# Performance work log

Hardware: AMD Instinct MI355X
Metric: run time of the kernel (lower is better)

The kernel has to match this reference:

```python
import jax, jax.numpy as jnp
import numpy as np

EPS = 1e-12  # matches torch F.normalize eps


def _l2_normalize(x, axis=-1):
    # torch.F.normalize: x / max(||x||, eps)
    n = jnp.sqrt(jnp.sum(x * x, axis=axis, keepdims=True))
    return x / jnp.maximum(n, EPS)


def setup_inputs() -> dict:
    N, n_classes, embed_dim = 32768, 1000, 1024
    key = jax.random.key(0)
    k_feat, k_lab, k_proto = jax.random.split(key, 3)

    features = jax.random.normal(k_feat, (N, embed_dim), dtype=jnp.float32)

    # one-hot float labels, as expected by `torch.matmul(labels, self.mean_class)`
    y = jax.random.randint(k_lab, (N,), 0, n_classes)
    labels = jax.nn.one_hot(y, n_classes, dtype=jnp.float32)

    # predefined prototypes: orthonormal rows (ortho_group.rvs equivalent via QR)
    g = jax.random.normal(k_proto, (embed_dim, embed_dim), dtype=jnp.float32)
    q, _ = jnp.linalg.qr(g)
    mean_class = q[:n_classes]  # [n_classes, embed_dim], orthonormal rows

    return {"features": features, "labels": labels, "mean_class": mean_class}


def reference(features, labels, mean_class):
    # features: [N, D]; labels: [N, C] one-hot; mean_class: [C, D]
    # (3-D feature mean-pooling branch not exercised: inputs are 2-D)
    proto_y = labels @ mean_class                 # [N, D]
    f = _l2_normalize(features, axis=1)
    p = _l2_normalize(proto_y, axis=1)
    # diag(f @ p.T) == rowwise dot product -> same math, O(N*D) not O(N^2*D)
    cos = jnp.einsum("nd,nd->n", f, p)            # [N]
    return jnp.mean(1.0 - cos)
```

## Files before the change

kernel.cpp:

```cpp
#include <hip/hip_runtime.h>

constexpr int N_CLASSES = 1000;
constexpr int EMBED     = 1024;

typedef float floatx4 __attribute__((ext_vector_type(4)));

__global__ __launch_bounds__(256) void angular_rows_kernel(
    const float* __restrict__ features,
    const float* __restrict__ labels,
    const float* __restrict__ mean_class,
    float* __restrict__ partials,
    int n_rows)
{
    const int tid  = threadIdx.x;
    const int lane = tid & 63;
    const int wave = tid >> 6;
    const int row  = blockIdx.x * 4 + wave;

    float res = 0.0f;

    if (row < n_rows) {
        const floatx4* frow = (const floatx4*)(features + (size_t)row * EMBED);
        floatx4 f0 = __builtin_nontemporal_load(frow + lane);
        floatx4 f1 = __builtin_nontemporal_load(frow + lane + 64);
        floatx4 f2 = __builtin_nontemporal_load(frow + lane + 128);
        floatx4 f3 = __builtin_nontemporal_load(frow + lane + 192);

        const floatx4* lrow = (const floatx4*)(labels + (size_t)row * N_CLASSES);
        floatx4 l0 = __builtin_nontemporal_load(lrow + lane);
        floatx4 l1 = __builtin_nontemporal_load(lrow + lane + 64);
        floatx4 l2 = __builtin_nontemporal_load(lrow + lane + 128);
        floatx4 l3 = (lane < N_CLASSES / 4 - 192)
                         ? __builtin_nontemporal_load(lrow + lane + 192)
                         : (floatx4){0.f, 0.f, 0.f, 0.f};

        int cand = -1;
        if (l0.x != 0.f) cand = 4 * lane + 0;
        if (l0.y != 0.f) cand = 4 * lane + 1;
        if (l0.z != 0.f) cand = 4 * lane + 2;
        if (l0.w != 0.f) cand = 4 * lane + 3;
        if (l1.x != 0.f) cand = 4 * (lane + 64) + 0;
        if (l1.y != 0.f) cand = 4 * (lane + 64) + 1;
        if (l1.z != 0.f) cand = 4 * (lane + 64) + 2;
        if (l1.w != 0.f) cand = 4 * (lane + 64) + 3;
        if (l2.x != 0.f) cand = 4 * (lane + 128) + 0;
        if (l2.y != 0.f) cand = 4 * (lane + 128) + 1;
        if (l2.z != 0.f) cand = 4 * (lane + 128) + 2;
        if (l2.w != 0.f) cand = 4 * (lane + 128) + 3;
        if (l3.x != 0.f) cand = 4 * (lane + 192) + 0;
        if (l3.y != 0.f) cand = 4 * (lane + 192) + 1;
        if (l3.z != 0.f) cand = 4 * (lane + 192) + 2;
        if (l3.w != 0.f) cand = 4 * (lane + 192) + 3;

        unsigned long long m = __ballot(cand >= 0);
        int src = __ffsll((unsigned long long)m) - 1;
        int cls = __shfl(cand, src, 64);
        cls = __builtin_amdgcn_readfirstlane(cls);

        const floatx4* prow = (const floatx4*)(mean_class + (size_t)cls * EMBED);
        floatx4 p0 = prow[lane];
        floatx4 p1 = prow[lane + 64];
        floatx4 p2 = prow[lane + 128];
        floatx4 p3 = prow[lane + 192];

        float ff = 0.f, pp = 0.f, fp = 0.f;
        #define DOT3(F, P) \
            ff += F.x*F.x + F.y*F.y + F.z*F.z + F.w*F.w; \
            pp += P.x*P.x + P.y*P.y + P.z*P.z + P.w*P.w; \
            fp += F.x*P.x + F.y*P.y + F.z*P.z + F.w*P.w;
        DOT3(f0, p0) DOT3(f1, p1) DOT3(f2, p2) DOT3(f3, p3)
        #undef DOT3

        #pragma unroll
        for (int msk = 1; msk < 64; msk <<= 1) {
            ff += __shfl_xor(ff, msk, 64);
            pp += __shfl_xor(pp, msk, 64);
            fp += __shfl_xor(fp, msk, 64);
        }
        const float denom = fmaxf(sqrtf(ff), 1e-12f) * fmaxf(sqrtf(pp), 1e-12f);
        res = 1.0f - fp / denom;
    }

    __shared__ float s_red[4];
    if (lane == 0) s_red[wave] = res;
    __syncthreads();
    if (tid == 0)
        partials[blockIdx.x] = s_red[0] + s_red[1] + s_red[2] + s_red[3];
}

__global__ __launch_bounds__(256) void reduce_partials_kernel(
    const float* __restrict__ partials, int num_partials,
    float* __restrict__ out, float inv_n)
{
    const int tid  = threadIdx.x;
    const int lane = tid & 63;
    const int wave = tid >> 6;
    __shared__ float s_red[4];

    float acc = 0.0f;
    for (int i = tid; i < num_partials; i += 256)
        acc += partials[i];
    #pragma unroll
    for (int msk = 1; msk < 64; msk <<= 1)
        acc += __shfl_xor(acc, msk, 64);
    if (lane == 0) s_red[wave] = acc;
    __syncthreads();
    if (tid == 0)
        out[0] = (s_red[0] + s_red[1] + s_red[2] + s_red[3]) * inv_n;
}

extern "C" void kernel_launch(void* const* d_in, const int* in_sizes, int n_in,
                              void* d_out, int out_size, void* d_ws, size_t ws_size,
                              hipStream_t stream) {
    const float* features   = (const float*)d_in[0];
    const float* labels     = (const float*)d_in[1];
    const float* mean_class = (const float*)d_in[2];
    float* out = (float*)d_out;
    float* partials = (float*)d_ws;

    const int n_rows = in_sizes[0] / EMBED;
    const int num_blocks = (n_rows + 3) / 4;

    angular_rows_kernel<<<num_blocks, 256, 0, stream>>>(
        features, labels, mean_class, partials, n_rows);
    reduce_partials_kernel<<<1, 256, 0, stream>>>(
        partials, num_blocks, out, 1.0f / (float)n_rows);
}
```

Before: 260.5 us.

## Split label class scan into separate kernel before dot-product kernel

Moves the one-hot label scan into its own kernel, with one block per row, that writes each row's class index to a workspace buffer. The dot-product kernel then reads that index and can issue the prototype loads alongside the feature loads, instead of waiting on the label load, ballot and shuffle chain. The cost is an extra kernel launch, a 32768-block grid in which 6 of every 256 threads sit idle, and a round trip of the index buffer through memory. If a label row is all zeros, its cls_buf entry is never written and holds whatever was left in the workspace.

```diff
diff --git a/kernel.cpp b/kernel.cpp
--- a/kernel.cpp
+++ b/kernel.cpp
@@ -5,10 +5,29 @@
 
 typedef float floatx4 __attribute__((ext_vector_type(4)));
 
-__global__ __launch_bounds__(256) void angular_rows_kernel(
+__global__ __launch_bounds__(256) void class_scan_kernel(
+    const float* __restrict__ labels,
+    int* __restrict__ cls_buf)
+{
+    const int row = blockIdx.x;
+    const int t   = threadIdx.x;
+    if (t < N_CLASSES / 4) {
+        const floatx4* lrow = (const floatx4*)(labels + (size_t)row * N_CLASSES);
+        floatx4 v = __builtin_nontemporal_load(lrow + t);
+        if (v.x != 0.f || v.y != 0.f || v.z != 0.f || v.w != 0.f) {
+            int c = 4 * t;
+            if      (v.y != 0.f) c += 1;
+            else if (v.z != 0.f) c += 2;
+            else if (v.w != 0.f) c += 3;
+            cls_buf[row] = c;
+        }
+    }
+}
+
+__global__ __launch_bounds__(256) void angular_dots_kernel(
     const float* __restrict__ features,
-    const float* __restrict__ labels,
     const float* __restrict__ mean_class,
+    const int* __restrict__ cls_buf,
     float* __restrict__ partials,
     int n_rows)
 {
@@ -20,44 +39,15 @@
     float res = 0.0f;
 
     if (row < n_rows) {
+        const int cls = __builtin_amdgcn_readfirstlane(cls_buf[row]);
+
         const floatx4* frow = (const floatx4*)(features + (size_t)row * EMBED);
+        const floatx4* prow = (const floatx4*)(mean_class + (size_t)cls * EMBED);
+
         floatx4 f0 = __builtin_nontemporal_load(frow + lane);
         floatx4 f1 = __builtin_nontemporal_load(frow + lane + 64);
         floatx4 f2 = __builtin_nontemporal_load(frow + lane + 128);
         floatx4 f3 = __builtin_nontemporal_load(frow + lane + 192);
-
-        const floatx4* lrow = (const floatx4*)(labels + (size_t)row * N_CLASSES);
-        floatx4 l0 = __builtin_nontemporal_load(lrow + lane);
-        floatx4 l1 = __builtin_nontemporal_load(lrow + lane + 64);
-        floatx4 l2 = __builtin_nontemporal_load(lrow + lane + 128);
-        floatx4 l3 = (lane < N_CLASSES / 4 - 192)
-                         ? __builtin_nontemporal_load(lrow + lane + 192)
-                         : (floatx4){0.f, 0.f, 0.f, 0.f};
-
-        int cand = -1;
-        if (l0.x != 0.f) cand = 4 * lane + 0;
-        if (l0.y != 0.f) cand = 4 * lane + 1;
-        if (l0.z != 0.f) cand = 4 * lane + 2;
-        if (l0.w != 0.f) cand = 4 * lane + 3;
-        if (l1.x != 0.f) cand = 4 * (lane + 64) + 0;
-        if (l1.y != 0.f) cand = 4 * (lane + 64) + 1;
-        if (l1.z != 0.f) cand = 4 * (lane + 64) + 2;
-        if (l1.w != 0.f) cand = 4 * (lane + 64) + 3;
-        if (l2.x != 0.f) cand = 4 * (lane + 128) + 0;
-        if (l2.y != 0.f) cand = 4 * (lane + 128) + 1;
-        if (l2.z != 0.f) cand = 4 * (lane + 128) + 2;
-        if (l2.w != 0.f) cand = 4 * (lane + 128) + 3;
-        if (l3.x != 0.f) cand = 4 * (lane + 192) + 0;
-        if (l3.y != 0.f) cand = 4 * (lane + 192) + 1;
-        if (l3.z != 0.f) cand = 4 * (lane + 192) + 2;
-        if (l3.w != 0.f) cand = 4 * (lane + 192) + 3;
-
-        unsigned long long m = __ballot(cand >= 0);
-        int src = __ffsll((unsigned long long)m) - 1;
-        int cls = __shfl(cand, src, 64);
-        cls = __builtin_amdgcn_readfirstlane(cls);
-
-        const floatx4* prow = (const floatx4*)(mean_class + (size_t)cls * EMBED);
         floatx4 p0 = prow[lane];
         floatx4 p1 = prow[lane + 64];
         floatx4 p2 = prow[lane + 128];
@@ -116,13 +106,16 @@
     const float* labels     = (const float*)d_in[1];
     const float* mean_class = (const float*)d_in[2];
     float* out = (float*)d_out;
-    float* partials = (float*)d_ws;
 
     const int n_rows = in_sizes[0] / EMBED;
-    const int num_blocks = (n_rows + 3) / 4;
+    int* cls_buf    = (int*)d_ws;
+    float* partials = (float*)d_ws + n_rows;
 
-    angular_rows_kernel<<<num_blocks, 256, 0, stream>>>(
-        features, labels, mean_class, partials, n_rows);
+    const int dot_blocks = (n_rows + 3) / 4;
+
+    class_scan_kernel<<<n_rows, 256, 0, stream>>>(labels, cls_buf);
+    angular_dots_kernel<<<dot_blocks, 256, 0, stream>>>(
+        features, mean_class, cls_buf, partials, n_rows);
     reduce_partials_kernel<<<1, 256, 0, stream>>>(
-        partials, num_blocks, out, 1.0f / (float)n_rows);
+        partials, dot_blocks, out, 1.0f / (float)n_rows);
 }
```

Result: no change. 260.8 us (+0.1%).

## Use persistent grid-stride waves with software-prefetched next row

Applied to the files above, without the earlier changes.

Replaces the one-row-per-wave launch with a fixed grid of 1024 blocks where each wave loops over rows in grid-stride order. While it processes the current row, it prefetches the next row's features and labels into registers. The label scan also tests each float4 once before finding the nonzero element. This is meant to overlap memory latency with compute and cut launch and tail overhead, at the cost of extra register pressure from double buffering and possibly lower occupancy.

```diff
diff --git a/kernel.cpp b/kernel.cpp
--- a/kernel.cpp
+++ b/kernel.cpp
@@ -5,7 +5,11 @@
 
 typedef float floatx4 __attribute__((ext_vector_type(4)));
 
-__global__ __launch_bounds__(256) void angular_rows_kernel(
+__device__ __forceinline__ floatx4 ntload(const floatx4* p) {
+    return __builtin_nontemporal_load(p);
+}
+
+__global__ __launch_bounds__(256, 4) void angular_pipelined_kernel(
     const float* __restrict__ features,
     const float* __restrict__ labels,
     const float* __restrict__ mean_class,
@@ -15,46 +19,53 @@
     const int tid  = threadIdx.x;
     const int lane = tid & 63;
     const int wave = tid >> 6;
-    const int row  = blockIdx.x * 4 + wave;
+    const int wave_id = (blockIdx.x * blockDim.x + tid) >> 6;
+    const int n_waves = (gridDim.x * blockDim.x) >> 6;
 
-    float res = 0.0f;
+    float acc = 0.0f;
 
-    if (row < n_rows) {
-        const floatx4* frow = (const floatx4*)(features + (size_t)row * EMBED);
-        floatx4 f0 = __builtin_nontemporal_load(frow + lane);
-        floatx4 f1 = __builtin_nontemporal_load(frow + lane + 64);
-        floatx4 f2 = __builtin_nontemporal_load(frow + lane + 128);
-        floatx4 f3 = __builtin_nontemporal_load(frow + lane + 192);
+    int r = wave_id;
+    floatx4 f0, f1, f2, f3, l0, l1, l2, l3;
+    if (r < n_rows) {
+        const floatx4* frow = (const floatx4*)(features + (size_t)r * EMBED);
+        f0 = ntload(frow + lane);       f1 = ntload(frow + lane + 64);
+        f2 = ntload(frow + lane + 128); f3 = ntload(frow + lane + 192);
+        const floatx4* lrow = (const floatx4*)(labels + (size_t)r * N_CLASSES);
+        l0 = ntload(lrow + lane);       l1 = ntload(lrow + lane + 64);
+        l2 = ntload(lrow + lane + 128);
+        l3 = (lane < N_CLASSES / 4 - 192) ? ntload(lrow + lane + 192)
+                                          : (floatx4){0.f, 0.f, 0.f, 0.f};
+    }
 
-        const floatx4* lrow = (const floatx4*)(labels + (size_t)row * N_CLASSES);
-        floatx4 l0 = __builtin_nontemporal_load(lrow + lane);
-        floatx4 l1 = __builtin_nontemporal_load(lrow + lane + 64);
-        floatx4 l2 = __builtin_nontemporal_load(lrow + lane + 128);
-        floatx4 l3 = (lane < N_CLASSES / 4 - 192)
-                         ? __builtin_nontemporal_load(lrow + lane + 192)
-                         : (floatx4){0.f, 0.f, 0.f, 0.f};
+    while (r < n_rows) {
+        const int rn = r + n_waves;
+        const bool has_next = rn < n_rows;
+        floatx4 nf0, nf1, nf2, nf3, nl0, nl1, nl2, nl3;
+        if (has_next) {
+            const floatx4* frow = (const floatx4*)(features + (size_t)rn * EMBED);
+            nf0 = ntload(frow + lane);       nf1 = ntload(frow + lane + 64);
+            nf2 = ntload(frow + lane + 128); nf3 = ntload(frow + lane + 192);
+            const floatx4* lrow = (const floatx4*)(labels + (size_t)rn * N_CLASSES);
+            nl0 = ntload(lrow + lane);       nl1 = ntload(lrow + lane + 64);
+            nl2 = ntload(lrow + lane + 128);
+            nl3 = (lane < N_CLASSES / 4 - 192) ? ntload(lrow + lane + 192)
+                                               : (floatx4){0.f, 0.f, 0.f, 0.f};
+        }
 
         int cand = -1;
-        if (l0.x != 0.f) cand = 4 * lane + 0;
-        if (l0.y != 0.f) cand = 4 * lane + 1;
-        if (l0.z != 0.f) cand = 4 * lane + 2;
-        if (l0.w != 0.f) cand = 4 * lane + 3;
-        if (l1.x != 0.f) cand = 4 * (lane + 64) + 0;
-        if (l1.y != 0.f) cand = 4 * (lane + 64) + 1;
-        if (l1.z != 0.f) cand = 4 * (lane + 64) + 2;
-        if (l1.w != 0.f) cand = 4 * (lane + 64) + 3;
-        if (l2.x != 0.f) cand = 4 * (lane + 128) + 0;
-        if (l2.y != 0.f) cand = 4 * (lane + 128) + 1;
-        if (l2.z != 0.f) cand = 4 * (lane + 128) + 2;
-        if (l2.w != 0.f) cand = 4 * (lane + 128) + 3;
-        if (l3.x != 0.f) cand = 4 * (lane + 192) + 0;
-        if (l3.y != 0.f) cand = 4 * (lane + 192) + 1;
-        if (l3.z != 0.f) cand = 4 * (lane + 192) + 2;
-        if (l3.w != 0.f) cand = 4 * (lane + 192) + 3;
+        #define SCAN(V, IDX) { \
+            if (V.x != 0.f || V.y != 0.f || V.z != 0.f || V.w != 0.f) { \
+                int c_ = 4 * (IDX); \
+                if      (V.y != 0.f) c_ += 1; \
+                else if (V.z != 0.f) c_ += 2; \
+                else if (V.w != 0.f) c_ += 3; \
+                cand = c_; \
+            } }
+        SCAN(l0, lane) SCAN(l1, lane + 64) SCAN(l2, lane + 128) SCAN(l3, lane + 192)
+        #undef SCAN
 
         unsigned long long m = __ballot(cand >= 0);
-        int src = __ffsll((unsigned long long)m) - 1;
-        int cls = __shfl(cand, src, 64);
+        int cls = __shfl(cand, __ffsll(m) - 1, 64);
         cls = __builtin_amdgcn_readfirstlane(cls);
 
         const floatx4* prow = (const floatx4*)(mean_class + (size_t)cls * EMBED);
@@ -77,12 +88,17 @@
             pp += __shfl_xor(pp, msk, 64);
             fp += __shfl_xor(fp, msk, 64);
         }
-        const float denom = fmaxf(sqrtf(ff), 1e-12f) * fmaxf(sqrtf(pp), 1e-12f);
-        res = 1.0f - fp / denom;
+        acc += 1.0f - fp / (fmaxf(sqrtf(ff), 1e-12f) * fmaxf(sqrtf(pp), 1e-12f));
+
+        r = rn;
+        if (has_next) {
+            f0 = nf0; f1 = nf1; f2 = nf2; f3 = nf3;
+            l0 = nl0; l1 = nl1; l2 = nl2; l3 = nl3;
+        }
     }
 
     __shared__ float s_red[4];
-    if (lane == 0) s_red[wave] = res;
+    if (lane == 0) s_red[wave] = acc;
     __syncthreads();
     if (tid == 0)
         partials[blockIdx.x] = s_red[0] + s_red[1] + s_red[2] + s_red[3];
@@ -119,9 +135,9 @@
     float* partials = (float*)d_ws;
 
     const int n_rows = in_sizes[0] / EMBED;
-    const int num_blocks = (n_rows + 3) / 4;
+    const int num_blocks = 1024;
 
-    angular_rows_kernel<<<num_blocks, 256, 0, stream>>>(
+    angular_pipelined_kernel<<<num_blocks, 256, 0, stream>>>(
         features, labels, mean_class, partials, n_rows);
     reduce_partials_kernel<<<1, 256, 0, stream>>>(
         partials, num_blocks, out, 1.0f / (float)n_rows);
```

Result: faster. 255.1 us (-2.1%).
